# Kernel tuning notes

Hardware: AMD Instinct MI355X
Metric: run time of the kernel (lower is better)

Reference implementation:

```python
import jax, jax.numpy as jnp
import numpy as np
import math

NUM_HEADS = 16
NUM_KV_HEADS = 4
HEAD_DIM = 128
HIDDEN = 2048
ROPE_BASE = 10000.0


def setup_inputs() -> dict:
    key = jax.random.key(0)
    ks = jax.random.split(key, 6)
    B, S = 1, 4096
    hidden_states = jax.random.normal(ks[0], (B, S, HIDDEN), dtype=jnp.float32)
    attention_mask = jnp.ones((B, S), dtype=jnp.int32)
    position_ids = jnp.broadcast_to(jnp.arange(S, dtype=jnp.int32)[None, :], (B, S))
    sc = 1.0 / math.sqrt(HIDDEN)
    wq = jax.random.normal(ks[1], (HIDDEN, NUM_HEADS * HEAD_DIM), dtype=jnp.float32) * sc
    wk = jax.random.normal(ks[2], (HIDDEN, NUM_KV_HEADS * HEAD_DIM), dtype=jnp.float32) * sc
    wv = jax.random.normal(ks[3], (HIDDEN, NUM_KV_HEADS * HEAD_DIM), dtype=jnp.float32) * sc
    wo = jax.random.normal(ks[4], (NUM_HEADS * HEAD_DIM, HIDDEN), dtype=jnp.float32) * sc
    return {"hidden_states": hidden_states, "attention_mask": attention_mask,
            "position_ids": position_ids, "wq": wq, "wk": wk, "wv": wv, "wo": wo}


def _rotate_half(x):
    x1, x2 = jnp.split(x, 2, axis=-1)
    return jnp.concatenate((-x2, x1), axis=-1)


def _rope_tables(seq_len, dtype):
    inv_freq = 1.0 / (ROPE_BASE ** (jnp.arange(0, HEAD_DIM, 2, dtype=jnp.float32) / HEAD_DIM))
    t = jnp.arange(seq_len, dtype=jnp.float32)
    freqs = jnp.outer(t, inv_freq)                       # [S, hd/2]
    emb = jnp.concatenate((freqs, freqs), axis=-1)       # [S, hd]
    return jnp.cos(emb).astype(dtype), jnp.sin(emb).astype(dtype)


def reference(hidden_states, attention_mask, position_ids, wq, wk, wv, wo):
    B, S, _ = hidden_states.shape
    dtype = hidden_states.dtype
    # projections -> [B, H, S, hd]
    q = (hidden_states @ wq).reshape(B, S, NUM_HEADS, HEAD_DIM).transpose(0, 2, 1, 3)
    k = (hidden_states @ wk).reshape(B, S, NUM_KV_HEADS, HEAD_DIM).transpose(0, 2, 1, 3)
    v = (hidden_states @ wv).reshape(B, S, NUM_KV_HEADS, HEAD_DIM).transpose(0, 2, 1, 3)
    # RoPE
    cos_t, sin_t = _rope_tables(S, dtype)
    cos = cos_t[position_ids][:, None]                   # [B,1,S,hd]
    sin = sin_t[position_ids][:, None]
    q = q * cos + _rotate_half(q) * sin
    k = k * cos + _rotate_half(k) * sin
    # GQA repeat
    n_rep = NUM_HEADS // NUM_KV_HEADS
    k = jnp.repeat(k, n_rep, axis=1)
    v = jnp.repeat(v, n_rep, axis=1)
    # scores + causal mask + padding mask
    scores = jnp.einsum('bhqd,bhkd->bhqk', q, k) / math.sqrt(HEAD_DIM)
    neg = jnp.finfo(scores.dtype).min
    causal = jnp.triu(jnp.full((S, S), neg, dtype=scores.dtype), k=1)
    scores = scores + causal[None, None]
    pad = (1.0 - attention_mask.astype(scores.dtype))[:, None, None, :] * neg
    scores = scores + pad
    attn = jax.nn.softmax(scores.astype(jnp.float32), axis=-1).astype(dtype)
    out = jnp.einsum('bhqk,bhkd->bhqd', attn, v)
    out = out.transpose(0, 2, 1, 3).reshape(B, S, NUM_HEADS * HEAD_DIM)
    return out @ wo
```

## Files before the change

kernel.cpp:

```cpp
#include <hip/hip_runtime.h>
#include <cstdint>
#include <cstddef>

typedef unsigned short ushort_t;
typedef short    bf16x8 __attribute__((ext_vector_type(8)));
typedef float    f32x4  __attribute__((ext_vector_type(4)));
typedef uint4    __attribute__((may_alias)) uint4_a;
typedef ushort4  __attribute__((may_alias)) ushort4_a;
typedef float4   __attribute__((may_alias)) float4_a;
typedef unsigned __attribute__((may_alias)) uint_a;

constexpr int SEQ = 4096, HID = 2048, NHEADS = 16, NKVH = 4, HDIM = 128;
constexpr int QD  = NHEADS * HDIM;
constexpr int KVD = NKVH * HDIM;
constexpr int KVL = 2 * KVD;

static __device__ __forceinline__ float bf2f(ushort_t u) {
    return __uint_as_float(((unsigned)u) << 16);
}
static __device__ __forceinline__ ushort_t f2bf(float f) {
    unsigned x = __float_as_uint(f);
    unsigned r = x + 0x7FFFu + ((x >> 16) & 1u);
    return (ushort_t)(r >> 16);
}
static __device__ __forceinline__ unsigned pack2(float lo, float hi) {
    return (unsigned)f2bf(lo) | ((unsigned)f2bf(hi) << 16);
}
static __device__ __forceinline__ unsigned cvt_pk(float lo, float hi) {
    unsigned r;
    asm("v_cvt_pk_bf16_f32 %0, %1, %2" : "=v"(r) : "v"(lo), "v"(hi));
    return r;
}

static __device__ __forceinline__ void gld16(const ushort_t* g, ushort_t* l) {
    __builtin_amdgcn_global_load_lds(
        (const __attribute__((address_space(1))) unsigned*)g,
        (__attribute__((address_space(3))) unsigned*)l, 16, 0, 0);
}

__global__ __launch_bounds__(256) void cast_f32_bf16(
    const float* __restrict__ in, ushort_t* __restrict__ out, int n)
{
    int i = (blockIdx.x * 256 + threadIdx.x) * 8;
    if (i >= n) return;
    float4 a = *(const float4_a*)(in + i);
    float4 b = *(const float4_a*)(in + i + 4);
    uint4 o;
    o.x = pack2(a.x, a.y); o.y = pack2(a.z, a.w);
    o.z = pack2(b.x, b.y); o.w = pack2(b.z, b.w);
    *(uint4_a*)(out + i) = o;
}

__global__ __launch_bounds__(256) void transpose_cast(
    const float* __restrict__ W, ushort_t* __restrict__ WT, int K, int N)
{
    __shared__ float tl[32][36];
    const int k0 = blockIdx.x * 32, n0 = blockIdx.y * 32;
    const int t  = threadIdx.x;
    {
        int i = t >> 3, jb = (t & 7) * 4;
        *(float4_a*)&tl[i][jb] = *(const float4_a*)(W + (size_t)(k0 + i) * N + n0 + jb);
    }
    __syncthreads();
    {
        int n = t >> 3, kb = (t & 7) * 4;
        ushort4 o;
        o.x = f2bf(tl[kb + 0][n]); o.y = f2bf(tl[kb + 1][n]);
        o.z = f2bf(tl[kb + 2][n]); o.w = f2bf(tl[kb + 3][n]);
        *(ushort4_a*)(WT + (size_t)(n0 + n) * K + k0 + kb) = o;
    }
}

__global__ __launch_bounds__(256) void gemm_mfma(
    const ushort_t* __restrict__ A, int lda,
    const ushort_t* __restrict__ Bt, int ldb,
    void* __restrict__ C1, int ld1, void* __restrict__ C2, int ld2,
    int split, int N, int K, int out_f32)
{
    __shared__ ushort_t as[128 * 32];
    __shared__ ushort_t bs[128 * 32];

    const int t    = threadIdx.x;
    const int mb   = blockIdx.y * 128, nb = blockIdx.x * 128;
    const int w    = t >> 6, lane = t & 63, quad = lane >> 4, l15 = lane & 15;
    const int wm   = (w >> 1) * 64, wn = (w & 1) * 64;

    const int dr_row = lane >> 2, dr_c = lane & 3;
    const int rA0 = w * 16 + dr_row, rA1 = 64 + w * 16 + dr_row;
    const ushort_t* a0p = A  + (size_t)(mb + rA0) * lda + (dr_c ^ (rA0 & 3)) * 8;
    const ushort_t* a1p = A  + (size_t)(mb + rA1) * lda + (dr_c ^ (rA1 & 3)) * 8;
    const ushort_t* b0p = Bt + (size_t)(nb + rA0) * ldb + (dr_c ^ (rA0 & 3)) * 8;
    const ushort_t* b1p = Bt + (size_t)(nb + rA1) * ldb + (dr_c ^ (rA1 & 3)) * 8;
    ushort_t* asb0 = &as[(w) * 512];        ushort_t* asb1 = &as[(4 + w) * 512];
    ushort_t* bsb0 = &bs[(w) * 512];        ushort_t* bsb1 = &bs[(4 + w) * 512];

    f32x4 acc[4][4];
#pragma unroll
    for (int i = 0; i < 4; i++)
#pragma unroll
        for (int j = 0; j < 4; j++) acc[i][j] = (f32x4)0.f;

    const int chunk = quad ^ (l15 & 3);

    for (int kb = 0; kb < K; kb += 32) {
        __syncthreads();
        gld16(a0p + kb, asb0);
        gld16(a1p + kb, asb1);
        gld16(b0p + kb, bsb0);
        gld16(b1p + kb, bsb1);
        __syncthreads();

        bf16x8 af[4], bf[4];
#pragma unroll
        for (int mt = 0; mt < 4; mt++)
            af[mt] = *(const bf16x8*)&as[(wm + mt * 16 + l15) * 32 + chunk * 8];
#pragma unroll
        for (int nt = 0; nt < 4; nt++)
            bf[nt] = *(const bf16x8*)&bs[(wn + nt * 16 + l15) * 32 + chunk * 8];
#pragma unroll
        for (int mt = 0; mt < 4; mt++)
#pragma unroll
            for (int nt = 0; nt < 4; nt++)
                acc[mt][nt] = __builtin_amdgcn_mfma_f32_16x16x32_bf16(
                    af[mt], bf[nt], acc[mt][nt], 0, 0, 0);
    }

#pragma unroll
    for (int mt = 0; mt < 4; mt++)
#pragma unroll
        for (int nt = 0; nt < 4; nt++) {
            int colg = nb + wn + nt * 16 + l15;
#pragma unroll
            for (int r = 0; r < 4; r++) {
                int row = mb + wm + mt * 16 + quad * 4 + r;
                float v = acc[mt][nt][r];
                if (out_f32)            ((float*)C1)[(size_t)row * ld1 + colg] = v;
                else if (colg < split)  ((ushort_t*)C1)[(size_t)row * ld1 + colg] = f2bf(v);
                else                    ((ushort_t*)C2)[(size_t)row * ld2 + colg - split] = f2bf(v);
            }
        }
}

__global__ __launch_bounds__(256) void rope_bf16(
    ushort_t* __restrict__ buf, int ld, int nh, const int* __restrict__ pos_ids)
{
    int idx  = blockIdx.x * 256 + threadIdx.x;
    int i    = idx & 63;
    int rem  = idx >> 6;
    int head = rem % nh;
    int s    = rem / nh;
    if (s >= SEQ) return;

    float pos = (float)pos_ids[s];
    float ang = pos * __expf(-(float)i * 0.14391156831212787f);
    float c, sn;
    sincosf(ang, &sn, &c);

    ushort_t* p = buf + (size_t)s * ld + head * HDIM;
    float x0 = bf2f(p[i]);
    float x1 = bf2f(p[i + 64]);
    p[i]      = f2bf(x0 * c - x1 * sn);
    p[i + 64] = f2bf(x1 * c + x0 * sn);
}

__global__ __launch_bounds__(512, 4) void flash_mfma(
    const ushort_t* Q, const ushort_t* __restrict__ KV,
    const int* __restrict__ amask, ushort_t* O)
{
    __shared__ ushort_t ks[64][136];
    __shared__ ushort_t vt[128][72];
    __shared__ float    bias[64];

    const int t = threadIdx.x, w = t >> 6, lane = t & 63;
    const int quad = lane >> 4, l15 = lane & 15;
    const int h = blockIdx.x, kvh = h >> 2;
    const int q0 = (31 - blockIdx.y) * 128;
    const int q0w = q0 + w * 16;
    const int kcol = kvh * HDIM, vcol = KVD + kvh * HDIM;
    const float scale2 = 0.08838834764831845f * 1.44269504088896340f;

    const int krow = t >> 3,  kdo = (t & 7) * 16;
    const int vkp  = t & 31,  vdg = t >> 5;

    int bpi[4];
#pragma unroll
    for (int t4 = 0; t4 < 4; t4++)
        bpi[t4] = ((2 * (quad & 1) + (t4 >> 1)) * 16 + l15) * 4;
    const bool hi_half = (quad >> 1) != 0;

    bf16x8 qf[4];
    {
        const ushort_t* qp = Q + (size_t)(q0w + l15) * QD + h * HDIM;
#pragma unroll
        for (int c = 0; c < 4; c++)
            qf[c] = *(const bf16x8*)(qp + c * 32 + quad * 8);
    }

    f32x4 accO[8];
#pragma unroll
    for (int j = 0; j < 8; j++) accO[j] = (f32x4)0.f;
    float m_s = -1e30f, l_s = 0.f;

    uint4 kst[2], va, vb;
    float bst = 0.f;
    auto stage_load = [&](int kt) {
        const int k0 = kt * 64;
        const ushort_t* kp = KV + (size_t)(k0 + krow) * KVL + kcol + kdo;
        kst[0] = *(const uint4_a*)kp;
        kst[1] = *(const uint4_a*)(kp + 8);
        const ushort_t* vp = KV + (size_t)(k0 + 2 * vkp) * KVL + vcol + vdg * 8;
        va = *(const uint4_a*)vp;
        vb = *(const uint4_a*)(vp + KVL);
        if (t < 64) bst = amask[k0 + t] ? 0.f : -1e30f;
    };

    const int nkt = (q0 >> 6) + 2;
    stage_load(0);

    for (int kt = 0; kt < nkt; kt++) {
        const int k0 = kt * 64;
        __syncthreads();
        *(uint4_a*)&ks[krow][kdo]     = kst[0];
        *(uint4_a*)&ks[krow][kdo + 8] = kst[1];
        {
            unsigned aw[4] = {va.x, va.y, va.z, va.w};
            unsigned bw[4] = {vb.x, vb.y, vb.z, vb.w};
#pragma unroll
            for (int i = 0; i < 4; i++) {
                *(uint_a*)&vt[vdg * 8 + 2 * i][2 * vkp] =
                    (aw[i] & 0xFFFFu) | (bw[i] << 16);
                *(uint_a*)&vt[vdg * 8 + 2 * i + 1][2 * vkp] =
                    (aw[i] >> 16) | (bw[i] & 0xFFFF0000u);
            }
        }
        if (t < 64) bias[t] = bst;
        __syncthreads();
        if (kt + 1 < nkt) stage_load(kt + 1);

        if (k0 > q0w + 15) continue;

        f32x4 s[4];
#pragma unroll
        for (int mt = 0; mt < 4; mt++) s[mt] = (f32x4)0.f;
#pragma unroll
        for (int c = 0; c < 4; c++)
#pragma unroll
            for (int mt = 0; mt < 4; mt++) {
                bf16x8 kf = *(const bf16x8*)&ks[mt * 16 + l15][c * 32 + quad * 8];
                s[mt] = __builtin_amdgcn_mfma_f32_16x16x32_bf16(kf, qf[c], s[mt], 0, 0, 0);
            }

        const int qg = q0w + l15;
        const bool full = (k0 + 63 <= q0w);
        float p[4][4];
        float mx = -1e30f;
#pragma unroll
        for (int mt = 0; mt < 4; mt++) {
            float4 b4 = *(const float4_a*)&bias[mt * 16 + quad * 4];
            float br[4] = {b4.x, b4.y, b4.z, b4.w};
#pragma unroll
            for (int r = 0; r < 4; r++) {
                float v = fmaf(s[mt][r], scale2, br[r]);
                if (!full) {
                    int kg = k0 + mt * 16 + quad * 4 + r;
                    v = (kg > qg) ? -1e30f : v;
                }
                p[mt][r] = v;
                mx = fmaxf(mx, v);
            }
        }
        mx = fmaxf(mx, __shfl_xor(mx, 16));
        mx = fmaxf(mx, __shfl_xor(mx, 32));
        const bool renorm = !__all(mx <= m_s + 8.f);
        const float mnew = renorm ? fmaxf(m_s, mx) : m_s;
        float sum = 0.f;
        unsigned wlo[4], whi[4];
#pragma unroll
        for (int mt = 0; mt < 4; mt++) {
            float p0 = exp2f(p[mt][0] - mnew);
            float p1 = exp2f(p[mt][1] - mnew);
            float p2 = exp2f(p[mt][2] - mnew);
            float p3 = exp2f(p[mt][3] - mnew);
            sum += (p0 + p1) + (p2 + p3);
            wlo[mt] = cvt_pk(p0, p1);
            whi[mt] = cvt_pk(p2, p3);
        }
        sum += __shfl_xor(sum, 16);
        sum += __shfl_xor(sum, 32);

        if (renorm) {
            float alpha = exp2f(m_s - mnew);
            l_s *= alpha;
            float a0 = __shfl(alpha, quad * 4 + 0);
            float a1 = __shfl(alpha, quad * 4 + 1);
            float a2 = __shfl(alpha, quad * 4 + 2);
            float a3 = __shfl(alpha, quad * 4 + 3);
#pragma unroll
            for (int j = 0; j < 8; j++) {
                f32x4 a = accO[j];
                a[0] *= a0; a[1] *= a1; a[2] *= a2; a[3] *= a3;
                accO[j] = a;
            }
        }
        m_s = mnew;
        l_s += sum;

#pragma unroll
        for (int kc = 0; kc < 2; kc++) {
            union { unsigned u[4]; bf16x8 v; } pf;
#pragma unroll
            for (int t4 = 0; t4 < 4; t4++) {
                unsigned slo = (t4 & 1) ? whi[2 * kc]     : wlo[2 * kc];
                unsigned shi = (t4 & 1) ? whi[2 * kc + 1] : wlo[2 * kc + 1];
                int ra = __builtin_amdgcn_ds_bpermute(bpi[t4], (int)slo);
                int rb = __builtin_amdgcn_ds_bpermute(bpi[t4], (int)shi);
                pf.u[t4] = (unsigned)(hi_half ? rb : ra);
            }
#pragma unroll
            for (int n8 = 0; n8 < 8; n8++) {
                bf16x8 vf = *(const bf16x8*)&vt[n8 * 16 + l15][kc * 32 + quad * 8];
                accO[n8] = __builtin_amdgcn_mfma_f32_16x16x32_bf16(pf.v, vf, accO[n8], 0, 0, 0);
            }
        }
    }

    float linv = 1.0f / l_s;
#pragma unroll
    for (int r = 0; r < 4; r++) {
        float lr = __shfl(linv, quad * 4 + r);
        int row = q0w + quad * 4 + r;
        ushort_t* op = O + (size_t)row * QD + h * HDIM;
#pragma unroll
        for (int n8 = 0; n8 < 8; n8++)
            op[n8 * 16 + l15] = f2bf(accO[n8][r] * lr);
    }
}

extern "C" void kernel_launch(void* const* d_in, const int* in_sizes, int n_in,
                              void* d_out, int out_size, void* d_ws, size_t ws_size,
                              hipStream_t stream)
{
    const float* x     = (const float*)d_in[0];
    const int*   amask = (const int*)d_in[1];
    const int*   pos   = (const int*)d_in[2];
    const float* wq    = (const float*)d_in[3];
    const float* wk    = (const float*)d_in[4];
    const float* wv    = (const float*)d_in[5];
    const float* wo    = (const float*)d_in[6];
    float* out = (float*)d_out;

    ushort_t* wqkvT = (ushort_t*)d_out;
    ushort_t* xb    = wqkvT + (size_t)3072 * HID;

    ushort_t* qbuf  = (ushort_t*)d_ws;
    ushort_t* kvbuf = qbuf + (size_t)SEQ * QD;
    ushort_t* woT   = kvbuf;

    cast_f32_bf16<<<SEQ * HID / 8 / 256, 256, 0, stream>>>(x, xb, SEQ * HID);
    transpose_cast<<<dim3(HID / 32, QD / 32),  256, 0, stream>>>(wq, wqkvT, HID, QD);
    transpose_cast<<<dim3(HID / 32, KVD / 32), 256, 0, stream>>>(wk, wqkvT + (size_t)QD * HID, HID, KVD);
    transpose_cast<<<dim3(HID / 32, KVD / 32), 256, 0, stream>>>(wv, wqkvT + (size_t)(QD + KVD) * HID, HID, KVD);

    gemm_mfma<<<dim3(3072 / 128, SEQ / 128), 256, 0, stream>>>(
        xb, HID, wqkvT, HID, qbuf, QD, kvbuf, KVL, QD, 3072, HID, 0);

    rope_bf16<<<SEQ * NHEADS * 64 / 256, 256, 0, stream>>>(qbuf, QD, NHEADS, pos);
    rope_bf16<<<SEQ * NKVH  * 64 / 256, 256, 0, stream>>>(kvbuf, KVL, NKVH, pos);

    flash_mfma<<<dim3(NHEADS, 32), 512, 0, stream>>>(qbuf, kvbuf, amask, qbuf);

    transpose_cast<<<dim3(QD / 32, HID / 32), 256, 0, stream>>>(wo, woT, QD, HID);
    gemm_mfma<<<dim3(HID / 128, SEQ / 128), 256, 0, stream>>>(
        qbuf, QD, woT, QD, out, HID, out, HID, HID, HID, QD, 1);
}
```

Measured before the change: 501.1 us.

## Split long causal query tiles across KV chunks and combine partials (split-K flash)

Query tiles 16-31 now have their KV range split into up to 4 chunks of 16 key tiles, each run by its own block. Each chunk writes unnormalized bf16 partial outputs plus per-row max and sum into scratch reused from the output buffer. A new combine kernel merges the chunks with log-sum-exp weights. Blocks are ordered so the longest chunks launch first, and launch bounds go from 4 to 8 waves per SIMD. The goal is to even out causal load imbalance and keep more CUs busy, at the cost of an extra kernel, partial-output traffic and some extra bf16 rounding.

```diff
diff --git a/kernel.cpp b/kernel.cpp
--- a/kernel.cpp
+++ b/kernel.cpp
@@ -8,12 +8,14 @@
 typedef uint4    __attribute__((may_alias)) uint4_a;
 typedef ushort4  __attribute__((may_alias)) ushort4_a;
 typedef float4   __attribute__((may_alias)) float4_a;
+typedef float2   __attribute__((may_alias)) float2_a;
 typedef unsigned __attribute__((may_alias)) uint_a;
 
 constexpr int SEQ = 4096, HID = 2048, NHEADS = 16, NKVH = 4, HDIM = 128;
 constexpr int QD  = NHEADS * HDIM;
 constexpr int KVD = NKVH * HDIM;
 constexpr int KVL = 2 * KVD;
+constexpr int NPART = 56;
 
 static __device__ __forceinline__ float bf2f(ushort_t u) {
     return __uint_as_float(((unsigned)u) << 16);
@@ -163,9 +165,10 @@
     p[i + 64] = f2bf(x1 * c + x0 * sn);
 }
 
-__global__ __launch_bounds__(512, 4) void flash_mfma(
+__global__ __launch_bounds__(512, 8) void flash_mfma(
     const ushort_t* Q, const ushort_t* __restrict__ KV,
-    const int* __restrict__ amask, ushort_t* O)
+    const int* __restrict__ amask, ushort_t* O,
+    ushort_t* __restrict__ Opart, float2* __restrict__ ML)
 {
     __shared__ ushort_t ks[64][136];
     __shared__ ushort_t vt[128][72];
@@ -174,10 +177,26 @@
     const int t = threadIdx.x, w = t >> 6, lane = t & 63;
     const int quad = lane >> 4, l15 = lane & 15;
     const int h = blockIdx.x, kvh = h >> 2;
-    const int q0 = (31 - blockIdx.y) * 128;
-    const int q0w = q0 + w * 16;
+    const int s = blockIdx.y;
     const int kcol = kvh * HDIM, vcol = KVD + kvh * HDIM;
     const float scale2 = 0.08838834764831845f * 1.44269504088896340f;
+
+    int tile, ktb, kte, pid;
+    bool multi;
+    if (s < 8)       { tile = 15 - s;        ktb = 0; kte = 2 * tile + 2; multi = false; pid = 0; }
+    else if (s < 64) {
+        int cs = s - 8;
+        int c;
+        if (cs < 24) { tile = 16 + cs / 3; c = cs - (tile - 16) * 3; }
+        else         { int d = cs - 24; tile = 24 + (d >> 2); c = d & 3; }
+        int nkt = 2 * tile + 2;
+        ktb = c * 16; kte = (ktb + 16 < nkt) ? ktb + 16 : nkt;
+        multi = true; pid = h * NPART + cs;
+    }
+    else             { tile = 7 - (s - 64);  ktb = 0; kte = 2 * tile + 2; multi = false; pid = 0; }
+
+    const int q0  = tile * 128;
+    const int q0w = q0 + w * 16;
 
     const int krow = t >> 3,  kdo = (t & 7) * 16;
     const int vkp  = t & 31,  vdg = t >> 5;
@@ -214,10 +233,9 @@
         if (t < 64) bst = amask[k0 + t] ? 0.f : -1e30f;
     };
 
-    const int nkt = (q0 >> 6) + 2;
-    stage_load(0);
-
-    for (int kt = 0; kt < nkt; kt++) {
+    stage_load(ktb);
+
+    for (int kt = ktb; kt < kte; kt++) {
         const int k0 = kt * 64;
         __syncthreads();
         *(uint4_a*)&ks[krow][kdo]     = kst[0];
@@ -235,19 +253,19 @@
         }
         if (t < 64) bias[t] = bst;
         __syncthreads();
-        if (kt + 1 < nkt) stage_load(kt + 1);
+        if (kt + 1 < kte) stage_load(kt + 1);
 
         if (k0 > q0w + 15) continue;
 
-        f32x4 s[4];
-#pragma unroll
-        for (int mt = 0; mt < 4; mt++) s[mt] = (f32x4)0.f;
+        f32x4 sx[4];
+#pragma unroll
+        for (int mt = 0; mt < 4; mt++) sx[mt] = (f32x4)0.f;
 #pragma unroll
         for (int c = 0; c < 4; c++)
 #pragma unroll
             for (int mt = 0; mt < 4; mt++) {
                 bf16x8 kf = *(const bf16x8*)&ks[mt * 16 + l15][c * 32 + quad * 8];
-                s[mt] = __builtin_amdgcn_mfma_f32_16x16x32_bf16(kf, qf[c], s[mt], 0, 0, 0);
+                sx[mt] = __builtin_amdgcn_mfma_f32_16x16x32_bf16(kf, qf[c], sx[mt], 0, 0, 0);
             }
 
         const int qg = q0w + l15;
@@ -260,7 +278,7 @@
             float br[4] = {b4.x, b4.y, b4.z, b4.w};
 #pragma unroll
             for (int r = 0; r < 4; r++) {
-                float v = fmaf(s[mt][r], scale2, br[r]);
+                float v = fmaf(sx[mt][r], scale2, br[r]);
                 if (!full) {
                     int kg = k0 + mt * 16 + quad * 4 + r;
                     v = (kg > qg) ? -1e30f : v;
@@ -324,15 +342,77 @@
         }
     }
 
-    float linv = 1.0f / l_s;
-#pragma unroll
-    for (int r = 0; r < 4; r++) {
-        float lr = __shfl(linv, quad * 4 + r);
-        int row = q0w + quad * 4 + r;
-        ushort_t* op = O + (size_t)row * QD + h * HDIM;
-#pragma unroll
-        for (int n8 = 0; n8 < 8; n8++)
-            op[n8 * 16 + l15] = f2bf(accO[n8][r] * lr);
+    if (!multi) {
+        float linv = 1.0f / l_s;
+#pragma unroll
+        for (int r = 0; r < 4; r++) {
+            float lr = __shfl(linv, quad * 4 + r);
+            int row = q0w + quad * 4 + r;
+            ushort_t* op = O + (size_t)row * QD + h * HDIM;
+#pragma unroll
+            for (int n8 = 0; n8 < 8; n8++)
+                op[n8 * 16 + l15] = f2bf(accO[n8][r] * lr);
+        }
+    } else {
+        ushort_t* op = Opart + (size_t)pid * (128 * 128);
+#pragma unroll
+        for (int r = 0; r < 4; r++) {
+            int row = w * 16 + quad * 4 + r;
+#pragma unroll
+            for (int n8 = 0; n8 < 8; n8++)
+                op[row * 128 + n8 * 16 + l15] = f2bf(accO[n8][r]);
+        }
+        if (quad == 0)
+            ML[pid * 128 + w * 16 + l15] = make_float2(m_s, l_s);
+    }
+}
+
+__global__ __launch_bounds__(256) void combine_partials(
+    const ushort_t* __restrict__ P, const float2* __restrict__ ML,
+    ushort_t* __restrict__ O)
+{
+    const int h = blockIdx.x >> 4, tt = blockIdx.x & 15, tile = 16 + tt;
+    const int nc = (tile < 24) ? 3 : 4;
+    const int pid0 = h * NPART + ((tile < 24) ? tt * 3 : 24 + (tile - 24) * 4);
+    const int tid = threadIdx.x;
+    const int row = tid >> 1, dh = (tid & 1) << 6;
+
+    float m_[4], l_[4];
+    float M = -1e30f;
+#pragma unroll
+    for (int c = 0; c < 4; c++) {
+        if (c < nc) {
+            float2 v = *(const float2_a*)&ML[(pid0 + c) * 128 + row];
+            m_[c] = v.x; l_[c] = v.y; M = fmaxf(M, v.x);
+        } else { m_[c] = -1e30f; l_[c] = 0.f; }
+    }
+    float L = 0.f, wgt[4];
+#pragma unroll
+    for (int c = 0; c < 4; c++) { wgt[c] = exp2f(m_[c] - M); L += wgt[c] * l_[c]; }
+    const float inv = 1.0f / L;
+
+    ushort_t* op = O + (size_t)(tile * 128 + row) * QD + h * HDIM + dh;
+    const size_t pbase = (size_t)row * 128 + dh;
+#pragma unroll
+    for (int g = 0; g < 8; g++) {
+        float acc[8] = {0.f, 0.f, 0.f, 0.f, 0.f, 0.f, 0.f, 0.f};
+#pragma unroll
+        for (int c = 0; c < 4; c++) {
+            if (c < nc) {
+                const ushort_t* pp = P + (size_t)(pid0 + c) * (128 * 128) + pbase + g * 8;
+                uint4 v = *(const uint4_a*)pp;
+                unsigned u[4] = {v.x, v.y, v.z, v.w};
+#pragma unroll
+                for (int j = 0; j < 4; j++) {
+                    acc[2 * j]     += wgt[c] * bf2f((ushort_t)(u[j] & 0xFFFFu));
+                    acc[2 * j + 1] += wgt[c] * bf2f((ushort_t)(u[j] >> 16));
+                }
+            }
+        }
+        uint4 o;
+        o.x = pack2(acc[0] * inv, acc[1] * inv); o.y = pack2(acc[2] * inv, acc[3] * inv);
+        o.z = pack2(acc[4] * inv, acc[5] * inv); o.w = pack2(acc[6] * inv, acc[7] * inv);
+        *(uint4_a*)(op + g * 8) = o;
     }
 }
 
@@ -356,6 +436,9 @@
     ushort_t* kvbuf = qbuf + (size_t)SEQ * QD;
     ushort_t* woT   = kvbuf;
 
+    ushort_t* opart = (ushort_t*)d_out;
+    float2*   mlbuf = (float2*)((char*)d_out + (size_t)16 * NPART * 128 * 128 * 2);
+
     cast_f32_bf16<<<SEQ * HID / 8 / 256, 256, 0, stream>>>(x, xb, SEQ * HID);
     transpose_cast<<<dim3(HID / 32, QD / 32),  256, 0, stream>>>(wq, wqkvT, HID, QD);
     transpose_cast<<<dim3(HID / 32, KVD / 32), 256, 0, stream>>>(wk, wqkvT + (size_t)QD * HID, HID, KVD);
@@ -367,7 +450,9 @@
     rope_bf16<<<SEQ * NHEADS * 64 / 256, 256, 0, stream>>>(qbuf, QD, NHEADS, pos);
     rope_bf16<<<SEQ * NKVH  * 64 / 256, 256, 0, stream>>>(kvbuf, KVL, NKVH, pos);
 
-    flash_mfma<<<dim3(NHEADS, 32), 512, 0, stream>>>(qbuf, kvbuf, amask, qbuf);
+    flash_mfma<<<dim3(NHEADS, 72), 512, 0, stream>>>(
+        qbuf, kvbuf, amask, qbuf, opart, mlbuf);
+    combine_partials<<<dim3(256), 256, 0, stream>>>(opart, mlbuf, qbuf);
 
     transpose_cast<<<dim3(QD / 32, HID / 32), 256, 0, stream>>>(wo, woT, QD, HID);
     gemm_mfma<<<dim3(HID / 128, SEQ / 128), 256, 0, stream>>>(
```

Measured after the change: 884.3 us. 1.76x slower.
